# Kernel tuning notes

Measured on AMD Instinct MI355X. Metric: run time of the kernel, lower is better.

Reference implementation:

```python
import jax, jax.numpy as jnp
import numpy as np

B, S, D, H = 2, 2048, 1024, 16
HW = D // H  # head width = 64
MASK_FILL = -100000000.0


def setup_inputs() -> dict:
    key0 = jax.random.key(0)
    ks = jax.random.split(key0, 12)
    inp = {
        "query": jax.random.normal(ks[0], (B, S, D), jnp.float32),
        "key": jax.random.normal(ks[1], (B, S, D), jnp.float32),
        "value": jax.random.normal(ks[2], (B, S, D), jnp.float32),
        # bool mask, True masks; broadcasts over batch and heads
        "mask": jax.random.randint(ks[3], (S, S), 0, 2).astype(jnp.bool_),
        # per-head projection kernels: (heads, head_width, d_in)
        "Wq": jax.random.normal(ks[4], (H, HW, D), jnp.float32) * 0.02,
        "bq": jnp.zeros((H, HW), jnp.float32),
        "Wk": jax.random.normal(ks[5], (H, HW, D), jnp.float32) * 0.02,
        "bk": jnp.zeros((H, HW), jnp.float32),
        "Wv": jax.random.normal(ks[6], (H, HW, D), jnp.float32) * 0.02,
        "bv": jnp.zeros((H, HW), jnp.float32),
        # collapse projector: contracts (heads, head_width) -> d_output
        "Wo": jax.random.normal(ks[7], (D, H, HW), jnp.float32) * 0.02,
        "bo": jnp.zeros((D,), jnp.float32),
    }
    return inp


def reference(query, key, value, mask, Wq, bq, Wk, bk, Wv, bv, Wo, bo):
    # head projections -> (b, h, s, w)
    q = jnp.einsum("bsd,hwd->bhsw", query, Wq) + bq[:, None, :]
    k = jnp.einsum("btd,hwd->bhtw", key, Wk) + bk[:, None, :]
    v = jnp.einsum("btd,hwd->bhtw", value, Wv) + bv[:, None, :]
    # unscaled logits, masked_fill, softmax (matches original exactly)
    logits = jnp.einsum("bhsw,bhtw->bhst", q, k)
    logits = jnp.where(mask, MASK_FILL, logits)
    score = jax.nn.softmax(logits, axis=-1)
    # NOTE: original divides AV output by sqrt(head_width) AFTER softmax
    attn = jnp.einsum("bhst,bhtw->bhsw", score, v) / jnp.sqrt(jnp.float32(HW))
    # collapse heads -> (b, s, d_output)
    out = jnp.einsum("bhsw,ohw->bso", attn, Wo) + bo
    return out
```

## Files before the change

kernel.cpp:

```cpp
#include <hip/hip_runtime.h>
#include <hip/hip_bf16.h>
#include <math.h>

#define S_LEN   2048
#define D_MODEL 1024
#define N_HEADS 16
#define HEAD_W  64
#define BATCH   2
#define MROWS   (BATCH * S_LEN)
#define MASK_FILL -100000000.0f
#define LOG2E 1.4426950408889634f

typedef __attribute__((ext_vector_type(8))) short bf16x8;
typedef __attribute__((ext_vector_type(4))) float f32x4;
typedef unsigned short u16;
typedef unsigned int   u32;
typedef unsigned long long u64;

__device__ __forceinline__ u16 f2bf(float f) {
    u32 u = __float_as_uint(f);
    return (u16)((u + 0x7fffu + ((u >> 16) & 1u)) >> 16);
}

__device__ __forceinline__ u32 pack_bf16x2(float lo, float hi) {
    __hip_bfloat162 t = __float22bfloat162_rn(make_float2(lo, hi));
    u32 r;
    __builtin_memcpy(&r, &t, 4);
    return r;
}

__device__ __forceinline__ void gld_lds16(const void* gp, void* lp) {
    __builtin_amdgcn_global_load_lds(
        (const __attribute__((address_space(1))) u32*)gp,
        (__attribute__((address_space(3))) u32*)lp, 16, 0, 0);
}

struct CvtJobs {
    const float* src[7];
    u16* dst[7];
    int n[7];
};
__global__ __launch_bounds__(256) void prep_kernel(
    CvtJobs j, const unsigned char* __restrict__ mask, u64* __restrict__ bits) {
    const int t = blockIdx.y;
    if (t < 7) {
        const float* s = j.src[t];
        u16* d = j.dst[t];
        const int n = j.n[t];
        int i = (blockIdx.x * 256 + threadIdx.x) * 4;
        if (i < n) {
            float4 v = *(const float4*)(s + i);
            ushort4 o;
            o.x = f2bf(v.x); o.y = f2bf(v.y); o.z = f2bf(v.z); o.w = f2bf(v.w);
            *(ushort4*)(d + i) = o;
        }
        return;
    }
    if (blockIdx.x >= 2048) return;
    __shared__ int isByte;
    if (threadIdx.x == 0) isByte = 0;
    __syncthreads();
    const int e0 = blockIdx.x * 2048;
    const uint2 v = ((const uint2*)(mask + e0))[threadIdx.x];
    if (((v.x | v.y) & 0xFFFFFF00u) != 0u) isByte = 1;
    __syncthreads();
    const int ib = isByte;
    const int* mi = (const int*)mask;
#pragma unroll
    for (int jj = 0; jj < 8; ++jj) {
        const int e = e0 + jj * 256 + threadIdx.x;
        const bool m = ib ? (mask[e] != 0) : (mi[e] != 0);
        const u64 bl = __ballot(m);
        if ((e & 63) == 0) bits[e >> 6] = bl;
    }
}

__device__ __forceinline__ void gemm_core_bf16(const u16* __restrict__ A,
                                               const u16* __restrict__ Bt,
                                               int m0, int n0, f32x4 acc[4][4]) {
    __shared__ u16 As[2][4096];
    __shared__ u16 Bs[2][4096];
    const int tid = threadIdx.x;
    const int wv = tid >> 6, ln = tid & 63;
    const int lane16 = ln & 15, quad = ln >> 4;
    const int wr = (wv >> 1) * 64, wc = (wv & 1) * 64;
    const u16* A0 = A + (size_t)(m0 + ln) * D_MODEL + wv * 8;
    const u16* A1 = A + (size_t)(m0 + 64 + ln) * D_MODEL + wv * 8;
    const u16* B0 = Bt + (size_t)(n0 + ln) * D_MODEL + wv * 8;
    const u16* B1 = Bt + (size_t)(n0 + 64 + ln) * D_MODEL + wv * 8;

    gld_lds16(A0, &As[0][wv * 1024]);
    gld_lds16(A1, &As[0][wv * 1024 + 512]);
    gld_lds16(B0, &Bs[0][wv * 1024]);
    gld_lds16(B1, &Bs[0][wv * 1024 + 512]);

    for (int kt = 0; kt < D_MODEL / 32; ++kt) {
        const int buf = kt & 1;
        __syncthreads();
        if (kt < D_MODEL / 32 - 1) {
            const int ko = (kt + 1) * 32;
            gld_lds16(A0 + ko, &As[buf ^ 1][wv * 1024]);
            gld_lds16(A1 + ko, &As[buf ^ 1][wv * 1024 + 512]);
            gld_lds16(B0 + ko, &Bs[buf ^ 1][wv * 1024]);
            gld_lds16(B1 + ko, &Bs[buf ^ 1][wv * 1024 + 512]);
        }
        bf16x8 af[4], bfv[4];
#pragma unroll
        for (int mt = 0; mt < 4; ++mt)
            af[mt] = *(const bf16x8*)&As[buf][quad * 1024 + (wr + mt * 16 + lane16) * 8];
#pragma unroll
        for (int nt = 0; nt < 4; ++nt)
            bfv[nt] = *(const bf16x8*)&Bs[buf][quad * 1024 + (wc + nt * 16 + lane16) * 8];
#pragma unroll
        for (int mt = 0; mt < 4; ++mt)
#pragma unroll
            for (int nt = 0; nt < 4; ++nt)
                acc[mt][nt] = __builtin_amdgcn_mfma_f32_16x16x32_bf16(
                    af[mt], bfv[nt], acc[mt][nt], 0, 0, 0);
    }
}

__global__ __launch_bounds__(256, 4) void qkv_gemm_kernel(
    const u16* __restrict__ xq, const u16* __restrict__ xk, const u16* __restrict__ xv,
    const u16* __restrict__ wq, const u16* __restrict__ wk, const u16* __restrict__ wv,
    const float* __restrict__ bq, const float* __restrict__ bk, const float* __restrict__ bv,
    u16* __restrict__ qb, u16* __restrict__ kb, u16* __restrict__ vtmp) {
    const u16* A; const u16* Bt; const float* bias; u16* outp;
    const int z = blockIdx.z;
    if (z == 0)      { A = xq; Bt = wq; bias = bq; outp = qb; }
    else if (z == 1) { A = xk; Bt = wk; bias = bk; outp = kb; }
    else             { A = xv; Bt = wv; bias = bv; outp = vtmp; }
    f32x4 acc[4][4] = {};
    const int m0 = blockIdx.y * 128, n0 = blockIdx.x * 128;
    gemm_core_bf16(A, Bt, m0, n0, acc);

    const int tid = threadIdx.x;
    const int wvi = tid >> 6, ln = tid & 63;
    const int lane16 = ln & 15, quad = ln >> 4;
    const int wr = (wvi >> 1) * 64, wc = (wvi & 1) * 64;
    const float scale = (z == 0) ? LOG2E : 1.0f;
#pragma unroll
    for (int nt = 0; nt < 4; ++nt) {
        const int n = n0 + wc + nt * 16 + lane16;
        const float bb = bias[n];
        const int h = n >> 6, w = n & 63;
#pragma unroll
        for (int mt = 0; mt < 4; ++mt)
#pragma unroll
            for (int r = 0; r < 4; ++r) {
                const int m = m0 + wr + mt * 16 + quad * 4 + r;
                const int bidx = m >> 11, s = m & 2047;
                outp[((size_t)((bidx * N_HEADS + h) * S_LEN + s)) * HEAD_W + w] =
                    f2bf((acc[mt][nt][r] + bb) * scale);
            }
    }
}

__global__ __launch_bounds__(256) void vtrans_kernel(
    const u16* __restrict__ vtmp, u16* __restrict__ vbt) {
    __shared__ u16 T[64][72];
    const int tid = threadIdx.x;
    const int bh = blockIdx.y;
    const int s0 = blockIdx.x * 64;
    const int row = tid >> 2, seg = (tid & 3) * 16;
    const u16* src = vtmp + ((size_t)bh * S_LEN + s0 + row) * HEAD_W + seg;
    uint4 a = *(const uint4*)src;
    uint4 b2 = *(const uint4*)(src + 8);
    u16 tmp[16];
    *(uint4*)tmp = a; *(uint4*)(tmp + 8) = b2;
#pragma unroll
    for (int j = 0; j < 16; ++j) T[seg + j][row] = tmp[j];
    __syncthreads();
    u16* dst = vbt + ((size_t)bh * HEAD_W + row) * S_LEN + s0 + seg;
    *(uint4*)dst       = *(const uint4*)&T[row][seg];
    *(uint4*)(dst + 8) = *(const uint4*)&T[row][seg + 8];
}

__global__ __launch_bounds__(256, 4) void out_gemm_kernel(
    const u16* __restrict__ ab, const u16* __restrict__ wo,
    const float* __restrict__ bo, float* __restrict__ out) {
    f32x4 acc[4][4] = {};
    const int m0 = blockIdx.y * 128, n0 = blockIdx.x * 128;
    gemm_core_bf16(ab, wo, m0, n0, acc);
    const int tid = threadIdx.x;
    const int wvi = tid >> 6, ln = tid & 63;
    const int lane16 = ln & 15, quad = ln >> 4;
    const int wr = (wvi >> 1) * 64, wc = (wvi & 1) * 64;
#pragma unroll
    for (int nt = 0; nt < 4; ++nt) {
        const int n = n0 + wc + nt * 16 + lane16;
        const float bb = bo[n];
#pragma unroll
        for (int mt = 0; mt < 4; ++mt)
#pragma unroll
            for (int r = 0; r < 4; ++r) {
                const int m = m0 + wr + mt * 16 + quad * 4 + r;
                out[(size_t)m * D_MODEL + n] = acc[mt][nt][r] + bb;
            }
    }
}

__global__ __launch_bounds__(256, 3) void attn_kernel(
    const u16* __restrict__ qbuf, const u16* __restrict__ kbuf,
    const u16* __restrict__ vbt, const u64* __restrict__ mbits,
    float* __restrict__ Opart, float* __restrict__ lpart) {
    __shared__ u16 Ks[2][4096];
    __shared__ u16 Vt[2][4096];
    __shared__ u16 Ps[4][32 * 72];
    const int tid = threadIdx.x;
    const int wv = tid >> 6, ln = tid & 63;
    const int lane16 = ln & 15, quad = ln >> 4;
    const int s_blk = blockIdx.x * 128;
    const int h = blockIdx.y;
    const int b = blockIdx.z >> 1, hf = blockIdx.z & 1;
    const int c0 = hf * 16;
    const size_t hb = ((size_t)(b * N_HEADS + h)) * S_LEN * HEAD_W;
    const u16* Qg = qbuf + hb;
    const u16* Kg = kbuf + hb;
    const u16* Vg = vbt + hb;

    bf16x8 qa[2][2];
#pragma unroll
    for (int mt = 0; mt < 2; ++mt)
#pragma unroll
        for (int kk = 0; kk < 2; ++kk)
            qa[mt][kk] = *(const bf16x8*)(Qg +
                (size_t)(s_blk + wv * 32 + mt * 16 + lane16) * HEAD_W + kk * 32 + quad * 8);

    const size_t mrow0 = (size_t)(s_blk + wv * 32 + lane16) * 32;
    const size_t mrow1 = (size_t)(s_blk + wv * 32 + 16 + lane16) * 32;
    u64 mwCur0 = mbits[mrow0 + c0], mwCur1 = mbits[mrow1 + c0];
    u64 mwNx0 = 0, mwNx1 = 0;

    {
        const int t0g = c0 * 64;
        const int i0 = 2 * wv, i1 = 2 * wv + 1;
        gld_lds16(Kg + (size_t)(t0g + ln) * HEAD_W + i0 * 8, &Ks[0][i0 * 512]);
        gld_lds16(Kg + (size_t)(t0g + ln) * HEAD_W + i1 * 8, &Ks[0][i1 * 512]);
        gld_lds16(Vg + (size_t)ln * S_LEN + t0g + i0 * 8, &Vt[0][i0 * 512]);
        gld_lds16(Vg + (size_t)ln * S_LEN + t0g + i1 * 8, &Vt[0][i1 * 512]);
    }

    f32x4 oacc[2][4] = {};
    float lsum[2] = {0.0f, 0.0f};

    for (int ci = 0; ci < 16; ++ci) {
        const int c = c0 + ci;
        const int buf = ci & 1;
        __syncthreads();
        if (ci < 15) {
            const int t1 = (c + 1) * 64;
            const int i0 = 2 * wv, i1 = 2 * wv + 1;
            gld_lds16(Kg + (size_t)(t1 + ln) * HEAD_W + i0 * 8, &Ks[buf ^ 1][i0 * 512]);
            gld_lds16(Kg + (size_t)(t1 + ln) * HEAD_W + i1 * 8, &Ks[buf ^ 1][i1 * 512]);
            gld_lds16(Vg + (size_t)ln * S_LEN + t1 + i0 * 8, &Vt[buf ^ 1][i0 * 512]);
            gld_lds16(Vg + (size_t)ln * S_LEN + t1 + i1 * 8, &Vt[buf ^ 1][i1 * 512]);
            mwNx0 = mbits[mrow0 + c + 1];
            mwNx1 = mbits[mrow1 + c + 1];
        }

        f32x4 st[4][2] = {};
#pragma unroll
        for (int kk = 0; kk < 2; ++kk)
#pragma unroll
            for (int ntT = 0; ntT < 4; ++ntT) {
                bf16x8 kf = *(const bf16x8*)&Ks[buf][(kk * 4 + quad) * 512 + (ntT * 16 + lane16) * 8];
#pragma unroll
                for (int mt = 0; mt < 2; ++mt)
                    st[ntT][mt] = __builtin_amdgcn_mfma_f32_16x16x32_bf16(
                        kf, qa[mt][kk], st[ntT][mt], 0, 0, 0);
            }

#pragma unroll
        for (int mt = 0; mt < 2; ++mt) {
            const u64 mw = mt ? mwCur1 : mwCur0;
            float ls0 = 0.0f, ls1 = 0.0f;
#pragma unroll
            for (int ntT = 0; ntT < 4; ++ntT) {
                const u32 nib = (u32)(mw >> (ntT * 16 + quad * 4)) & 15u;
                float p0 = exp2f(st[ntT][mt][0]); if (nib & 1u) p0 = 0.0f;
                float p1 = exp2f(st[ntT][mt][1]); if (nib & 2u) p1 = 0.0f;
                float p2 = exp2f(st[ntT][mt][2]); if (nib & 4u) p2 = 0.0f;
                float p3 = exp2f(st[ntT][mt][3]); if (nib & 8u) p3 = 0.0f;
                ls0 += p0 + p1;
                ls1 += p2 + p3;
                uint2 pk;
                pk.x = pack_bf16x2(p0, p1);
                pk.y = pack_bf16x2(p2, p3);
                *(uint2*)&Ps[wv][(mt * 16 + lane16) * 72 + ntT * 16 + quad * 4] = pk;
            }
            lsum[mt] += ls0 + ls1;
        }

        bf16x8 pf[2][2];
#pragma unroll
        for (int mt = 0; mt < 2; ++mt)
#pragma unroll
            for (int kk = 0; kk < 2; ++kk)
                pf[mt][kk] = *(const bf16x8*)&Ps[wv][(mt * 16 + lane16) * 72 + kk * 32 + quad * 8];
#pragma unroll
        for (int kk = 0; kk < 2; ++kk)
#pragma unroll
            for (int ntw = 0; ntw < 4; ++ntw) {
                bf16x8 vf = *(const bf16x8*)&Vt[buf][(kk * 4 + quad) * 512 + (ntw * 16 + lane16) * 8];
#pragma unroll
                for (int mt = 0; mt < 2; ++mt)
                    oacc[mt][ntw] = __builtin_amdgcn_mfma_f32_16x16x32_bf16(
                        pf[mt][kk], vf, oacc[mt][ntw], 0, 0, 0);
            }
        mwCur0 = mwNx0; mwCur1 = mwNx1;
    }

    float* OpB = Opart + ((size_t)(hf * 4096 + b * 2048)) * 1024;
#pragma unroll
    for (int mt = 0; mt < 2; ++mt) {
#pragma unroll
        for (int r = 0; r < 4; ++r) {
            const int s = s_blk + wv * 32 + mt * 16 + quad * 4 + r;
            float* dst = OpB + (size_t)s * 1024 + h * 64;
#pragma unroll
            for (int ntw = 0; ntw < 4; ++ntw)
                dst[ntw * 16 + lane16] = oacc[mt][ntw][r];
        }
        float lm = lsum[mt];
        lm += __shfl_xor(lm, 16);
        lm += __shfl_xor(lm, 32);
        if (quad == 0) {
            const int srow = s_blk + wv * 32 + mt * 16 + lane16;
            lpart[(size_t)(hf * 4096 + b * 2048 + srow) * 16 + h] = lm;
        }
    }
}

__global__ __launch_bounds__(256) void combine_kernel(
    const float* __restrict__ Op, const float* __restrict__ lp,
    u16* __restrict__ ab) {
    const int idx4 = blockIdx.x * 256 + threadIdx.x;
    const int row = idx4 >> 8;
    const int d = (idx4 & 255) * 4;
    const int h = d >> 6;
    const float l = lp[(size_t)row * 16 + h] + lp[(size_t)(4096 + row) * 16 + h];
    const float inv = 0.125f / l;
    float4 a = *(const float4*)(Op + (size_t)row * 1024 + d);
    float4 b = *(const float4*)(Op + (size_t)(4096 + row) * 1024 + d);
    ushort4 o;
    o.x = f2bf((a.x + b.x) * inv);
    o.y = f2bf((a.y + b.y) * inv);
    o.z = f2bf((a.z + b.z) * inv);
    o.w = f2bf((a.w + b.w) * inv);
    *(ushort4*)(ab + (size_t)row * 1024 + d) = o;
}

extern "C" void kernel_launch(void* const* d_in, const int* in_sizes, int n_in,
                              void* d_out, int out_size, void* d_ws, size_t ws_size,
                              hipStream_t stream) {
    const float* query = (const float*)d_in[0];
    const float* key   = (const float*)d_in[1];
    const float* value = (const float*)d_in[2];
    const void*  mask  = d_in[3];
    const float* Wq = (const float*)d_in[4];
    const float* bq = (const float*)d_in[5];
    const float* Wk = (const float*)d_in[6];
    const float* bk = (const float*)d_in[7];
    const float* Wv = (const float*)d_in[8];
    const float* bv = (const float*)d_in[9];
    const float* Wo = (const float*)d_in[10];
    const float* bo = (const float*)d_in[11];
    float* out = (float*)d_out;

    char* ws = (char*)d_ws;
    const size_t MB = 1024 * 1024;
    u64* bits = (u64*)ws;
    u16* wob  = (u16*)(ws + 1 * MB);
    u16* qb   = (u16*)(ws + 3 * MB);
    u16* kb   = (u16*)(ws + 11 * MB);
    u16* vbt  = (u16*)(ws + 19 * MB);
    char* uA = ws + 27 * MB;
    u16* xq   = (u16*)(uA);
    u16* xk   = (u16*)(uA + 8 * MB);
    u16* xv   = (u16*)(uA + 16 * MB);
    u16* wqb  = (u16*)(uA + 24 * MB);
    u16* wkb  = (u16*)(uA + 26 * MB);
    u16* wvb  = (u16*)(uA + 28 * MB);
    u16* vtmp = (u16*)(uA + 30 * MB);
    float* Opart = (float*)(uA);
    float* lpart = (float*)(uA + 32 * MB);
    u16* ab = qb;

    const size_t NACT = (size_t)MROWS * D_MODEL;
    const size_t NW   = (size_t)D_MODEL * D_MODEL;

    CvtJobs j;
    j.src[0] = query; j.dst[0] = xq;  j.n[0] = (int)NACT;
    j.src[1] = key;   j.dst[1] = xk;  j.n[1] = (int)NACT;
    j.src[2] = value; j.dst[2] = xv;  j.n[2] = (int)NACT;
    j.src[3] = Wq;    j.dst[3] = wqb; j.n[3] = (int)NW;
    j.src[4] = Wk;    j.dst[4] = wkb; j.n[4] = (int)NW;
    j.src[5] = Wv;    j.dst[5] = wvb; j.n[5] = (int)NW;
    j.src[6] = Wo;    j.dst[6] = wob; j.n[6] = (int)NW;
    prep_kernel<<<dim3(NACT / 1024, 8), 256, 0, stream>>>(
        j, (const unsigned char*)mask, bits);

    qkv_gemm_kernel<<<dim3(D_MODEL / 128, MROWS / 128, 3), 256, 0, stream>>>(
        xq, xk, xv, wqb, wkb, wvb, bq, bk, bv, qb, kb, vtmp);
    vtrans_kernel<<<dim3(S_LEN / 64, BATCH * N_HEADS), 256, 0, stream>>>(vtmp, vbt);
    attn_kernel<<<dim3(S_LEN / 128, N_HEADS, BATCH * 2), 256, 0, stream>>>(
        qb, kb, vbt, bits, Opart, lpart);
    combine_kernel<<<4096, 256, 0, stream>>>(Opart, lpart, ab);
    out_gemm_kernel<<<dim3(D_MODEL / 128, MROWS / 128), 256, 0, stream>>>(
        ab, wob, bo, out);
}
```

Before: 314.4 us.

## Precompute per-wave mask ballots, use scalar cndmask, MFMA row sums, swizzle blocks

Adds a kernel that rearranges the mask bits into per-wave 64-bit lane masks, so the attention softmax applies the mask with an inline-asm v_cndmask whose condition comes from a scalar register. The per-lane nibble extraction and the per-row mask loads go away. Row sums of P are now computed with an extra MFMA against a ones vector instead of VALU adds and shuffles. Workgroup IDs are remapped to change the order in which blocks are scheduled, and hardware exp2/rcp builtins replace the library calls. This adds a small extra kernel launch and extra MFMA work, and the inline asm depends on the ballot layout being exactly right.

```diff
diff --git a/kernel.cpp b/kernel.cpp
--- a/kernel.cpp
+++ b/kernel.cpp
@@ -17,6 +17,22 @@
 typedef unsigned int   u32;
 typedef unsigned long long u64;
 
+__device__ __forceinline__ float fast_exp2(float x) {
+#if __has_builtin(__builtin_amdgcn_exp2f)
+    return __builtin_amdgcn_exp2f(x);
+#else
+    return __builtin_exp2f(x);
+#endif
+}
+
+__device__ __forceinline__ float fast_rcp(float x) {
+#if __has_builtin(__builtin_amdgcn_rcpf)
+    return __builtin_amdgcn_rcpf(x);
+#else
+    return 1.0f / x;
+#endif
+}
+
 __device__ __forceinline__ u16 f2bf(float f) {
     u32 u = __float_as_uint(f);
     return (u16)((u + 0x7fffu + ((u >> 16) & 1u)) >> 16);
@@ -33,6 +49,12 @@
     __builtin_amdgcn_global_load_lds(
         (const __attribute__((address_space(1))) u32*)gp,
         (__attribute__((address_space(3))) u32*)lp, 16, 0, 0);
+}
+
+__device__ __forceinline__ float maskz(float p, u64 w) {
+    float r;
+    asm("v_cndmask_b32 %0, %1, 0, %2" : "=v"(r) : "v"(p), "s"(w));
+    return r;
 }
 
 struct CvtJobs {
@@ -75,6 +97,27 @@
     }
 }
 
+__global__ __launch_bounds__(256) void maskt_kernel(
+    const u64* __restrict__ bits, u64* __restrict__ words) {
+    const int tid = threadIdx.x, wv = tid >> 6, ln = tid & 63;
+    const int lane16 = ln & 15, quad = ln >> 4;
+    const int sg = blockIdx.x;
+#pragma unroll
+    for (int ci = 0; ci < 8; ++ci) {
+        const int c = wv * 8 + ci;
+        const u64 rw = bits[(size_t)(sg * 16 + lane16) * 32 + c];
+        u64 keep = 0;
+#pragma unroll
+        for (int k = 0; k < 16; ++k) {
+            const int ntT = k >> 2, r = k & 3;
+            const bool m = ((rw >> (ntT * 16 + quad * 4 + r)) & 1ull) != 0ull;
+            const u64 bl = __ballot(m);
+            if (ln == k) keep = bl;
+        }
+        if (ln < 16) words[(((size_t)sg * 32 + c) << 4) + ln] = keep;
+    }
+}
+
 __device__ __forceinline__ void gemm_core_bf16(const u16* __restrict__ A,
                                                const u16* __restrict__ Bt,
                                                int m0, int n0, f32x4 acc[4][4]) {
@@ -202,7 +245,7 @@
 
 __global__ __launch_bounds__(256, 3) void attn_kernel(
     const u16* __restrict__ qbuf, const u16* __restrict__ kbuf,
-    const u16* __restrict__ vbt, const u64* __restrict__ mbits,
+    const u16* __restrict__ vbt, const u64* __restrict__ maskw,
     float* __restrict__ Opart, float* __restrict__ lpart) {
     __shared__ u16 Ks[2][4096];
     __shared__ u16 Vt[2][4096];
@@ -210,14 +253,19 @@
     const int tid = threadIdx.x;
     const int wv = tid >> 6, ln = tid & 63;
     const int lane16 = ln & 15, quad = ln >> 4;
-    const int s_blk = blockIdx.x * 128;
-    const int h = blockIdx.y;
-    const int b = blockIdx.z >> 1, hf = blockIdx.z & 1;
+    const int fid = (blockIdx.z * N_HEADS + blockIdx.y) * (S_LEN / 128) + blockIdx.x;
+    const int nid = (fid & 7) * 128 + (fid >> 3);
+    const int s_blk = (nid & 15) * 128;
+    const int rest = nid >> 4;
+    const int h = rest & 15;
+    const int bz = rest >> 4;
+    const int b = bz >> 1, hf = bz & 1;
     const int c0 = hf * 16;
     const size_t hb = ((size_t)(b * N_HEADS + h)) * S_LEN * HEAD_W;
     const u16* Qg = qbuf + hb;
     const u16* Kg = kbuf + hb;
     const u16* Vg = vbt + hb;
+    const int sg0 = (s_blk >> 4) + wv * 2;
 
     bf16x8 qa[2][2];
 #pragma unroll
@@ -226,11 +274,6 @@
         for (int kk = 0; kk < 2; ++kk)
             qa[mt][kk] = *(const bf16x8*)(Qg +
                 (size_t)(s_blk + wv * 32 + mt * 16 + lane16) * HEAD_W + kk * 32 + quad * 8);
-
-    const size_t mrow0 = (size_t)(s_blk + wv * 32 + lane16) * 32;
-    const size_t mrow1 = (size_t)(s_blk + wv * 32 + 16 + lane16) * 32;
-    u64 mwCur0 = mbits[mrow0 + c0], mwCur1 = mbits[mrow1 + c0];
-    u64 mwNx0 = 0, mwNx1 = 0;
 
     {
         const int t0g = c0 * 64;
@@ -241,8 +284,12 @@
         gld_lds16(Vg + (size_t)ln * S_LEN + t0g + i1 * 8, &Vt[0][i1 * 512]);
     }
 
+    bf16x8 ones;
+#pragma unroll
+    for (int i = 0; i < 8; ++i) ones[i] = (short)0x3F80;
+
     f32x4 oacc[2][4] = {};
-    float lsum[2] = {0.0f, 0.0f};
+    f32x4 lacc[2] = {};
 
     for (int ci = 0; ci < 16; ++ci) {
         const int c = c0 + ci;
@@ -255,8 +302,6 @@
             gld_lds16(Kg + (size_t)(t1 + ln) * HEAD_W + i1 * 8, &Ks[buf ^ 1][i1 * 512]);
             gld_lds16(Vg + (size_t)ln * S_LEN + t1 + i0 * 8, &Vt[buf ^ 1][i0 * 512]);
             gld_lds16(Vg + (size_t)ln * S_LEN + t1 + i1 * 8, &Vt[buf ^ 1][i1 * 512]);
-            mwNx0 = mbits[mrow0 + c + 1];
-            mwNx1 = mbits[mrow1 + c + 1];
         }
 
         f32x4 st[4][2] = {};
@@ -273,23 +318,19 @@
 
 #pragma unroll
         for (int mt = 0; mt < 2; ++mt) {
-            const u64 mw = mt ? mwCur1 : mwCur0;
-            float ls0 = 0.0f, ls1 = 0.0f;
+            const u64* __restrict__ wp = maskw +
+                __builtin_amdgcn_readfirstlane((((sg0 + mt) * 32 + c) << 4));
 #pragma unroll
             for (int ntT = 0; ntT < 4; ++ntT) {
-                const u32 nib = (u32)(mw >> (ntT * 16 + quad * 4)) & 15u;
-                float p0 = exp2f(st[ntT][mt][0]); if (nib & 1u) p0 = 0.0f;
-                float p1 = exp2f(st[ntT][mt][1]); if (nib & 2u) p1 = 0.0f;
-                float p2 = exp2f(st[ntT][mt][2]); if (nib & 4u) p2 = 0.0f;
-                float p3 = exp2f(st[ntT][mt][3]); if (nib & 8u) p3 = 0.0f;
-                ls0 += p0 + p1;
-                ls1 += p2 + p3;
+                const float p0 = maskz(fast_exp2(st[ntT][mt][0]), wp[ntT * 4 + 0]);
+                const float p1 = maskz(fast_exp2(st[ntT][mt][1]), wp[ntT * 4 + 1]);
+                const float p2 = maskz(fast_exp2(st[ntT][mt][2]), wp[ntT * 4 + 2]);
+                const float p3 = maskz(fast_exp2(st[ntT][mt][3]), wp[ntT * 4 + 3]);
                 uint2 pk;
                 pk.x = pack_bf16x2(p0, p1);
                 pk.y = pack_bf16x2(p2, p3);
                 *(uint2*)&Ps[wv][(mt * 16 + lane16) * 72 + ntT * 16 + quad * 4] = pk;
             }
-            lsum[mt] += ls0 + ls1;
         }
 
         bf16x8 pf[2][2];
@@ -299,7 +340,11 @@
             for (int kk = 0; kk < 2; ++kk)
                 pf[mt][kk] = *(const bf16x8*)&Ps[wv][(mt * 16 + lane16) * 72 + kk * 32 + quad * 8];
 #pragma unroll
-        for (int kk = 0; kk < 2; ++kk)
+        for (int kk = 0; kk < 2; ++kk) {
+#pragma unroll
+            for (int mt = 0; mt < 2; ++mt)
+                lacc[mt] = __builtin_amdgcn_mfma_f32_16x16x32_bf16(
+                    pf[mt][kk], ones, lacc[mt], 0, 0, 0);
 #pragma unroll
             for (int ntw = 0; ntw < 4; ++ntw) {
                 bf16x8 vf = *(const bf16x8*)&Vt[buf][(kk * 4 + quad) * 512 + (ntw * 16 + lane16) * 8];
@@ -308,7 +353,7 @@
                     oacc[mt][ntw] = __builtin_amdgcn_mfma_f32_16x16x32_bf16(
                         pf[mt][kk], vf, oacc[mt][ntw], 0, 0, 0);
             }
-        mwCur0 = mwNx0; mwCur1 = mwNx1;
+        }
     }
 
     float* OpB = Opart + ((size_t)(hf * 4096 + b * 2048)) * 1024;
@@ -322,12 +367,12 @@
             for (int ntw = 0; ntw < 4; ++ntw)
                 dst[ntw * 16 + lane16] = oacc[mt][ntw][r];
         }
-        float lm = lsum[mt];
-        lm += __shfl_xor(lm, 16);
-        lm += __shfl_xor(lm, 32);
-        if (quad == 0) {
-            const int srow = s_blk + wv * 32 + mt * 16 + lane16;
-            lpart[(size_t)(hf * 4096 + b * 2048 + srow) * 16 + h] = lm;
+        if (lane16 == 0) {
+#pragma unroll
+            for (int r = 0; r < 4; ++r) {
+                const int srow = s_blk + wv * 32 + mt * 16 + quad * 4 + r;
+                lpart[(size_t)(hf * 4096 + b * 2048 + srow) * 16 + h] = lacc[mt][r];
+            }
         }
     }
 }
@@ -340,7 +385,7 @@
     const int d = (idx4 & 255) * 4;
     const int h = d >> 6;
     const float l = lp[(size_t)row * 16 + h] + lp[(size_t)(4096 + row) * 16 + h];
-    const float inv = 0.125f / l;
+    const float inv = 0.125f * fast_rcp(l);
     float4 a = *(const float4*)(Op + (size_t)row * 1024 + d);
     float4 b = *(const float4*)(Op + (size_t)(4096 + row) * 1024 + d);
     ushort4 o;
@@ -370,7 +415,8 @@
 
     char* ws = (char*)d_ws;
     const size_t MB = 1024 * 1024;
-    u64* bits = (u64*)ws;
+    u64* bits  = (u64*)ws;
+    u64* maskt = (u64*)(ws + 512 * 1024);
     u16* wob  = (u16*)(ws + 1 * MB);
     u16* qb   = (u16*)(ws + 3 * MB);
     u16* kb   = (u16*)(ws + 11 * MB);
@@ -400,12 +446,13 @@
     j.src[6] = Wo;    j.dst[6] = wob; j.n[6] = (int)NW;
     prep_kernel<<<dim3(NACT / 1024, 8), 256, 0, stream>>>(
         j, (const unsigned char*)mask, bits);
+    maskt_kernel<<<dim3(128), 256, 0, stream>>>(bits, maskt);
 
     qkv_gemm_kernel<<<dim3(D_MODEL / 128, MROWS / 128, 3), 256, 0, stream>>>(
         xq, xk, xv, wqb, wkb, wvb, bq, bk, bv, qb, kb, vtmp);
     vtrans_kernel<<<dim3(S_LEN / 64, BATCH * N_HEADS), 256, 0, stream>>>(vtmp, vbt);
     attn_kernel<<<dim3(S_LEN / 128, N_HEADS, BATCH * 2), 256, 0, stream>>>(
-        qb, kb, vbt, bits, Opart, lpart);
+        qb, kb, vbt, maskt, Opart, lpart);
     combine_kernel<<<4096, 256, 0, stream>>>(Opart, lpart, ab);
     out_gemm_kernel<<<dim3(D_MODEL / 128, MROWS / 128), 256, 0, stream>>>(
         ab, wob, bo, out);
```

After: 302.5 us. 1.04x faster.
